# Kernel tuning notes

Measured on AMD Instinct MI355X. Metric: run time of the kernel, lower is better.

## Reference

```python
import jax, jax.numpy as jnp
import numpy as np

B, N, D = 2, 8192, 32
RADIUS2 = 0.03 ** 2
SIM_THRESH = 0.7
MIN_LEAF = 10
EPS = 1e-8


def setup_inputs() -> dict:
    key = jax.random.key(0)
    ks = jax.random.split(key, 5)
    # points scaled to [0, 0.4)^3 so the 0.03 radius finds a few neighbors per point
    points = jax.random.uniform(ks[0], (B, N, 3), dtype=jnp.float32) * 0.4
    embeddings = jax.random.normal(ks[1], (B, N, D), dtype=jnp.float32)
    leaf_mask = jax.random.randint(ks[2], (B, N), 0, 2).astype(jnp.int32)
    # consistency_net: Linear(2D -> D), ReLU, Linear(D -> D); stored as (in, out)
    W1 = jax.random.normal(ks[3], (2 * D, D), dtype=jnp.float32) / np.sqrt(2 * D)
    b1 = jnp.zeros((D,), dtype=jnp.float32)
    W2 = jax.random.normal(ks[4], (D, D), dtype=jnp.float32) / np.sqrt(D)
    b2 = jnp.zeros((D,), dtype=jnp.float32)
    return {"points": points, "embeddings": embeddings, "leaf_mask": leaf_mask,
            "W1": W1, "b1": b1, "W2": W2, "b2": b2}


def reference(points, embeddings, leaf_mask, W1, b1, W2, b2):
    leaf = leaf_mask > 0  # [B,N]
    # squared pairwise distances via ||a||^2 + ||b||^2 - 2 a.b (avoids [B,N,N,3])
    sq = jnp.sum(points * points, axis=-1)  # [B,N]
    d2 = sq[:, :, None] + sq[:, None, :] - 2.0 * jnp.einsum('bnc,bmc->bnm', points, points)
    nb = (d2 < RADIUS2) & leaf[:, None, :]  # neighbor j must be a leaf point
    nb_count = jnp.sum(nb, axis=-1)  # includes self when leaf[i]
    # cosine similarity with per-vector norm clamp (torch F.cosine_similarity eps)
    norms = jnp.maximum(jnp.linalg.norm(embeddings, axis=-1, keepdims=True), EPS)
    en = embeddings / norms
    sim = jnp.einsum('bnd,bmd->bnm', en, en)
    similar = nb & (sim > SIM_THRESH)
    cnt = jnp.sum(similar, axis=-1)  # [B,N]
    w = similar.astype(embeddings.dtype)
    mean_sim = jnp.einsum('bnm,bmd->bnd', w, embeddings) / jnp.maximum(cnt, 1)[..., None]
    combined = jnp.concatenate([embeddings, mean_sim], axis=-1)  # [B,N,2D]
    h = jax.nn.relu(combined @ W1 + b1)
    out = h @ W2 + b2
    batch_ok = (jnp.sum(leaf, axis=-1) >= MIN_LEAF)[:, None]  # skip batches with <10 leaves
    cond = leaf & (nb_count > 1) & (cnt > 0) & batch_ok
    return jnp.where(cond[..., None], out, embeddings)
```

## Files before the change

kernel.cpp:

```cpp
#include <hip/hip_runtime.h>

#define NPTS 8192
#define BN   16384
#define D    32
#define R2   0.0009f
#define SIMT 0.7f
#define RAD  0.03f
#define BLOCK 256
#define PBLOCK 1024
#define PWAVES 16
#define NGRP   (BN / 64)
#define ZBINS 512
#define ZSCALE 1280.0f
#define AFIELDS 34
#define CHUNK 512

#define GLOBAL_AS __attribute__((address_space(1)))
#define LDS_AS    __attribute__((address_space(3)))

__device__ __forceinline__ void g2lds16(const void* g, void* l) {
  __builtin_amdgcn_global_load_lds((const GLOBAL_AS void*)g, (LDS_AS void*)l,
                                   16, 0, 0);
}

__global__ __launch_bounds__(BLOCK) void prep_kernel(
    const float* __restrict__ pts, const float* __restrict__ emb,
    const int* __restrict__ leaf,
    int* __restrict__ histA, int* __restrict__ histL,
    unsigned* __restrict__ done,
    int* __restrict__ rsA, int* __restrict__ rsL,
    int* __restrict__ curA, int* __restrict__ curL,
    float4* __restrict__ sortedA, int* __restrict__ permA,
    float4* __restrict__ pts4L, float* __restrict__ invL,
    float* __restrict__ embL) {
  const int p = blockIdx.x * BLOCK + threadIdx.x;
  const float x = pts[3 * p + 0];
  const float y = pts[3 * p + 1];
  const float z = pts[3 * p + 2];
  const float sq = x * x + y * y + z * z;
  int bin = (int)(z * ZSCALE); if (bin > ZBINS - 1) bin = ZBINS - 1;
  const int b = p >> 13;
  const int lf = leaf[p] > 0;
  atomicAdd(&histA[b * ZBINS + bin], 1);
  if (lf) atomicAdd(&histL[b * ZBINS + bin], 1);

  float4 er[D / 4];
  float ss = 0.f;
  {
    const float4* __restrict__ e4 = (const float4*)(emb + (size_t)p * D);
#pragma unroll
    for (int i = 0; i < D / 4; ++i) {
      er[i] = e4[i];
      ss += er[i].x * er[i].x + er[i].y * er[i].y +
            er[i].z * er[i].z + er[i].w * er[i].w;
    }
  }
  const float inv = 1.0f / fmaxf(sqrtf(ss), 1e-8f);

  __shared__ int islast;
  __threadfence();
  if (threadIdx.x == 0) {
    const unsigned t = __hip_atomic_fetch_add(&done[0], 1u, __ATOMIC_ACQ_REL,
                                              __HIP_MEMORY_SCOPE_AGENT);
    islast = (t == gridDim.x - 1);
  }
  __syncthreads();

  if (islast) {
    const int wv = threadIdx.x >> 6;
    const int lane = threadIdx.x & 63;
    const int sb = wv & 1;
    const int* __restrict__ h = (wv < 2) ? histA : histL;
    int* __restrict__ rs = (wv < 2) ? rsA : rsL;
    int* __restrict__ cu = (wv < 2) ? curA : curL;
    int carry = 0;
    for (int c = 0; c < ZBINS / 64; ++c) {
      const int idx = c * 64 + lane;
      const int v = __hip_atomic_load(&h[sb * ZBINS + idx], __ATOMIC_RELAXED,
                                      __HIP_MEMORY_SCOPE_AGENT);
      int incl = v;
#pragma unroll
      for (int off = 1; off < 64; off <<= 1) {
        const int t = __shfl_up(incl, off);
        if (lane >= off) incl += t;
      }
      const int excl = carry + incl - v;
      rs[sb * (ZBINS + 1) + idx] = excl;
      cu[sb * ZBINS + idx] = excl;
      carry += __shfl(incl, 63);
    }
    if (lane == 0) rs[sb * (ZBINS + 1) + ZBINS] = carry;
    __threadfence();
    __syncthreads();
    if (threadIdx.x == 0)
      __hip_atomic_store(&done[1], 1u, __ATOMIC_RELEASE,
                         __HIP_MEMORY_SCOPE_AGENT);
  } else {
    if (threadIdx.x == 0) {
      while (__hip_atomic_load(&done[1], __ATOMIC_ACQUIRE,
                               __HIP_MEMORY_SCOPE_AGENT) == 0)
        __builtin_amdgcn_s_sleep(8);
    }
    __syncthreads();
  }

  const int dst = b * NPTS + atomicAdd(&curA[b * ZBINS + bin], 1);
  sortedA[dst] = make_float4(x, y, z, lf ? inv : -inv);
  permA[dst] = p;

  if (lf) {
    const int dl = b * NPTS + atomicAdd(&curL[b * ZBINS + bin], 1);
    pts4L[dl] = make_float4(x, y, z, 0.5f * (sq - R2));
    invL[dl] = inv;
    float4* __restrict__ d4 = (float4*)(embL + (size_t)dl * D);
#pragma unroll
    for (int k = 0; k < D / 4; ++k) d4[k] = er[k];
  }
}

__global__ __launch_bounds__(PBLOCK) void pair_kernel(
    const float4* __restrict__ sortedA, const int* __restrict__ permA,
    const float4* __restrict__ pts4L, const float* __restrict__ invL,
    const float* __restrict__ embL, const float* __restrict__ emb,
    const int* __restrict__ rsL,
    const float* __restrict__ W1, const float* __restrict__ b1,
    const float* __restrict__ W2, const float* __restrict__ b2,
    float* __restrict__ out) {
  const int ig   = blockIdx.x;
  const int b    = ig >> 7;
  const int lane = threadIdx.x & 63;
  const int wv   = threadIdx.x >> 6;
  const int sg   = ig * 64 + lane;

  __shared__ __align__(16) float4 ptsS[2][CHUNK];
  __shared__ __align__(16) float4 eiS4[64 * 8];
  __shared__ float invIS[64];
  __shared__ int   queueS[PWAVES][128];
  __shared__ float red[AFIELDS][64];
  for (int t = threadIdx.x; t < AFIELDS * 64; t += PBLOCK)
    (&red[0][0])[t] = 0.f;

  const float4 A = sortedA[sg];
  const float inv_i = fabsf(A.w);
  const float mhsq = -0.5f * (A.x * A.x + A.y * A.y + A.z * A.z);
  const int p = permA[sg];

  if (wv == 0) {
    const float4* __restrict__ e4 = (const float4*)(emb + (size_t)p * D);
#pragma unroll
    for (int k = 0; k < D / 4; ++k) eiS4[lane * 8 + (k ^ (lane & 7))] = e4[k];
    invIS[lane] = inv_i;
  }

  float zmin = A.z, zmax = A.z;
#pragma unroll
  for (int off = 1; off < 64; off <<= 1) {
    zmin = fminf(zmin, __shfl_xor(zmin, off));
    zmax = fmaxf(zmax, __shfl_xor(zmax, off));
  }
  int klo = (int)((zmin - RAD) * ZSCALE) - 1; if (klo < 0) klo = 0;
  int khi = (int)((zmax + RAD) * ZSCALE) + 1; if (khi > ZBINS - 1) khi = ZBINS - 1;
  klo = __builtin_amdgcn_readfirstlane(klo);
  khi = __builtin_amdgcn_readfirstlane(khi);
  const int jlo = b * NPTS + rsL[b * (ZBINS + 1) + klo];
  const int jhi = b * NPTS + rsL[b * (ZBINS + 1) + khi + 1];
  const int len = jhi - jlo;

  float nbc = 0.f;
  int qtail = 0, qdone = 0;

  const float4* __restrict__ embQ = (const float4*)embL;

  auto drain = [&](int n) {
    if (lane < n) {
      const int e  = queueS[wv][(qdone + lane) & 127];
      const int il = e & 63;
      const int j  = e >> 6;
      float4 bv[D / 4];
#pragma unroll
      for (int k = 0; k < D / 4; ++k) bv[k] = embQ[(size_t)j * 8 + k];
      const float invj = invL[j];
      float s0 = 0.f, s1 = 0.f, s2 = 0.f, s3 = 0.f;
#pragma unroll
      for (int k = 0; k < D / 4; ++k) {
        const float4 av = eiS4[il * 8 + (k ^ (il & 7))];
        s0 = fmaf(av.x, bv[k].x, s0);
        s1 = fmaf(av.y, bv[k].y, s1);
        s2 = fmaf(av.z, bv[k].z, s2);
        s3 = fmaf(av.w, bv[k].w, s3);
      }
      const float sim = ((s0 + s1) + (s2 + s3)) * invIS[il] * invj;
      if (sim > SIMT) {
        atomicAdd(&red[1][il], 1.0f);
#pragma unroll
        for (int k = 0; k < D / 4; ++k) {
          atomicAdd(&red[2 + 4 * k + 0][il], bv[k].x);
          atomicAdd(&red[2 + 4 * k + 1][il], bv[k].y);
          atomicAdd(&red[2 + 4 * k + 2][il], bv[k].z);
          atomicAdd(&red[2 + 4 * k + 3][il], bv[k].w);
        }
      }
    }
    qdone += n;
  };

  auto stage = [&](int buf, int base, int L) {
    for (int t0 = wv * 64; t0 < L; t0 += PWAVES * 64)
      g2lds16((const char*)pts4L + (((size_t)(base + t0 + lane)) << 4),
              &ptsS[buf][t0]);
  };

  auto process = [&](int buf, int jbase, int L) {
    const int s0 = (L * wv) / PWAVES;
    const int s1 = (L * (wv + 1)) / PWAVES;
    if (s0 >= s1) return;
    float4 c = ptsS[buf][s0];
    for (int jl = s0; jl < s1; ++jl) {
      const float4 cn = ptsS[buf][(jl + 1 < s1) ? (jl + 1) : s0];
      const float t = fmaf(A.z, c.z, fmaf(A.y, c.y, fmaf(A.x, c.x, mhsq)));
      const bool hit = t > c.w;
      const unsigned long long m = __ballot(hit);
      if (m) {
        if (hit) {
          nbc += 1.0f;
          const int below = __popcll(m & ((1ull << lane) - 1ull));
          queueS[wv][(qtail + below) & 127] = ((jbase + jl) << 6) | lane;
        }
        qtail += (int)__popcll(m);
        if (qtail - qdone >= 64) drain(64);
      }
      c = cn;
    }
  };

  const int nch = (len + CHUNK - 1) / CHUNK;
  if (nch > 0) stage(0, jlo, (len < CHUNK) ? len : CHUNK);
  __syncthreads();
  for (int k = 0; k < nch; ++k) {
    const int cur = k & 1;
    if (k + 1 < nch) {
      const int base = jlo + (k + 1) * CHUNK;
      const int L = (jhi - base < CHUNK) ? (jhi - base) : CHUNK;
      stage(cur ^ 1, base, L);
    }
    const int base = jlo + k * CHUNK;
    const int Lc = (jhi - base < CHUNK) ? (jhi - base) : CHUNK;
    process(cur, base, Lc);
    __syncthreads();
  }
  drain(qtail - qdone);

  if (nbc != 0.f) atomicAdd(&red[0][lane], nbc);
  __syncthreads();

  if (threadIdx.x < 64) {
    const float tnbc = red[0][lane];
    const float tcnt = red[1][lane];
    const float rinv = 1.0f / fmaxf(tcnt, 1.0f);

    float e[D];
#pragma unroll
    for (int k = 0; k < D / 4; ++k) {
      const float4 v = eiS4[lane * 8 + (k ^ (lane & 7))];
      e[4 * k + 0] = v.x; e[4 * k + 1] = v.y;
      e[4 * k + 2] = v.z; e[4 * k + 3] = v.w;
    }

    float h[D];
#pragma unroll
    for (int k = 0; k < D; ++k) h[k] = b1[k];
    for (int d = 0; d < D; ++d) {
      const float c = e[d];
      const float* __restrict__ w = W1 + (size_t)d * D;
#pragma unroll
      for (int k = 0; k < D; ++k) h[k] = fmaf(c, w[k], h[k]);
    }
    for (int d = 0; d < D; ++d) {
      const float c = red[2 + d][lane] * rinv;
      const float* __restrict__ w = W1 + (size_t)(D + d) * D;
#pragma unroll
      for (int k = 0; k < D; ++k) h[k] = fmaf(c, w[k], h[k]);
    }
#pragma unroll
    for (int k = 0; k < D; ++k) h[k] = fmaxf(h[k], 0.f);

    float o[D];
#pragma unroll
    for (int m = 0; m < D; ++m) o[m] = b2[m];
    for (int k = 0; k < D; ++k) {
      const float c = h[k];
      const float* __restrict__ w = W2 + (size_t)k * D;
#pragma unroll
      for (int m = 0; m < D; ++m) o[m] = fmaf(c, w[m], o[m]);
    }

    const bool lf = A.w > 0.f;
    const int nleaf = rsL[b * (ZBINS + 1) + ZBINS];
    const bool cond = lf && (tnbc >= 2.0f) && (tcnt >= 1.0f) && (nleaf >= 10);

    float4* outr = (float4*)(out + (size_t)p * D);
#pragma unroll
    for (int i = 0; i < D / 4; ++i) {
      float4 v;
      if (cond) { v.x = o[4*i+0]; v.y = o[4*i+1]; v.z = o[4*i+2]; v.w = o[4*i+3]; }
      else      { v.x = e[4*i+0]; v.y = e[4*i+1]; v.z = e[4*i+2]; v.w = e[4*i+3]; }
      outr[i] = v;
    }
  }
}

extern "C" void kernel_launch(void* const* d_in, const int* in_sizes, int n_in,
                              void* d_out, int out_size, void* d_ws, size_t ws_size,
                              hipStream_t stream) {
  (void)in_sizes; (void)n_in; (void)out_size; (void)ws_size;
  const float* pts  = (const float*)d_in[0];
  const float* emb  = (const float*)d_in[1];
  const int*   leaf = (const int*)d_in[2];
  const float* W1   = (const float*)d_in[3];
  const float* b1   = (const float*)d_in[4];
  const float* W2   = (const float*)d_in[5];
  const float* b2   = (const float*)d_in[6];
  float* out = (float*)d_out;

  char* ws = (char*)d_ws;
  size_t off = 0;
  auto alloc = [&](size_t bytes) { void* r = ws + off; off = (off + bytes + 15) & ~(size_t)15; return r; };

  float4*   sortedA = (float4*)alloc((size_t)BN * 16);
  int*      permA   = (int*)alloc((size_t)BN * 4);
  float4*   pts4L   = (float4*)alloc((size_t)(BN + CHUNK) * 16);
  float*    invL    = (float*)alloc((size_t)(BN + CHUNK) * 4);
  float*    embL    = (float*)alloc((size_t)(BN + CHUNK) * D * 4);
  int*      rsA     = (int*)alloc(2 * (ZBINS + 1) * 4);
  int*      rsL     = (int*)alloc(2 * (ZBINS + 1) * 4);
  int*      curA    = (int*)alloc(2 * ZBINS * 4);
  int*      curL    = (int*)alloc(2 * ZBINS * 4);
  int*      histA   = (int*)alloc(2 * ZBINS * 4);
  int*      histL   = (int*)alloc(2 * ZBINS * 4);
  unsigned* done    = (unsigned*)alloc(16);

  hipMemsetAsync(histA, 0, 2 * (2 * ZBINS * 4) + 16, stream);
  prep_kernel<<<BN / BLOCK, BLOCK, 0, stream>>>(
      pts, emb, leaf, histA, histL, done, rsA, rsL, curA, curL,
      sortedA, permA, pts4L, invL, embL);
  pair_kernel<<<NGRP, PBLOCK, 0, stream>>>(
      sortedA, permA, pts4L, invL, embL, emb, rsL,
      W1, b1, W2, b2, out);
}
```

Before: 117.6 us.

## Make pair kernel persistent with 32-point groups and two candidate rows per wave step

The pair kernel becomes persistent: a grid of 256 blocks pulls work items from a global atomic counter. Each work item is a group of 32 sorted query points instead of 64. Each wave tests two candidate rows per iteration, one per 32-lane half, so the narrower z-band still fills all 64 lanes of the ballot. This aims to cut wasted candidate scanning and balance load across blocks. Separately, the prep kernel's last-block detection swaps a threadfence plus acq_rel atomic for a block barrier plus relaxed atomic, which weakens the memory-ordering guarantees before the histogram scan.

```diff
diff --git a/kernel.cpp b/kernel.cpp
--- a/kernel.cpp
+++ b/kernel.cpp
@@ -9,7 +9,9 @@
 #define BLOCK 256
 #define PBLOCK 1024
 #define PWAVES 16
-#define NGRP   (BN / 64)
+#define PGRID  256
+#define ISZ    32
+#define NGRP2  (BN / ISZ)
 #define ZBINS 512
 #define ZSCALE 1280.0f
 #define AFIELDS 34
@@ -58,9 +60,9 @@
   const float inv = 1.0f / fmaxf(sqrtf(ss), 1e-8f);
 
   __shared__ int islast;
-  __threadfence();
+  __syncthreads();
   if (threadIdx.x == 0) {
-    const unsigned t = __hip_atomic_fetch_add(&done[0], 1u, __ATOMIC_ACQ_REL,
+    const unsigned t = __hip_atomic_fetch_add(&done[0], 1u, __ATOMIC_RELAXED,
                                               __HIP_MEMORY_SCOPE_AGENT);
     islast = (t == gridDim.x - 1);
   }
@@ -125,186 +127,195 @@
     const int* __restrict__ rsL,
     const float* __restrict__ W1, const float* __restrict__ b1,
     const float* __restrict__ W2, const float* __restrict__ b2,
-    float* __restrict__ out) {
-  const int ig   = blockIdx.x;
-  const int b    = ig >> 7;
+    int* __restrict__ gctr, float* __restrict__ out) {
   const int lane = threadIdx.x & 63;
   const int wv   = threadIdx.x >> 6;
-  const int sg   = ig * 64 + lane;
+  const int il   = lane & 31;
+  const int rp   = lane >> 5;
 
   __shared__ __align__(16) float4 ptsS[2][CHUNK];
-  __shared__ __align__(16) float4 eiS4[64 * 8];
-  __shared__ float invIS[64];
+  __shared__ __align__(16) float4 eiS4[ISZ * 8];
+  __shared__ float invIS[ISZ];
   __shared__ int   queueS[PWAVES][128];
-  __shared__ float red[AFIELDS][64];
-  for (int t = threadIdx.x; t < AFIELDS * 64; t += PBLOCK)
-    (&red[0][0])[t] = 0.f;
-
-  const float4 A = sortedA[sg];
-  const float inv_i = fabsf(A.w);
-  const float mhsq = -0.5f * (A.x * A.x + A.y * A.y + A.z * A.z);
-  const int p = permA[sg];
-
-  if (wv == 0) {
-    const float4* __restrict__ e4 = (const float4*)(emb + (size_t)p * D);
-#pragma unroll
-    for (int k = 0; k < D / 4; ++k) eiS4[lane * 8 + (k ^ (lane & 7))] = e4[k];
-    invIS[lane] = inv_i;
-  }
-
-  float zmin = A.z, zmax = A.z;
-#pragma unroll
-  for (int off = 1; off < 64; off <<= 1) {
-    zmin = fminf(zmin, __shfl_xor(zmin, off));
-    zmax = fmaxf(zmax, __shfl_xor(zmax, off));
-  }
-  int klo = (int)((zmin - RAD) * ZSCALE) - 1; if (klo < 0) klo = 0;
-  int khi = (int)((zmax + RAD) * ZSCALE) + 1; if (khi > ZBINS - 1) khi = ZBINS - 1;
-  klo = __builtin_amdgcn_readfirstlane(klo);
-  khi = __builtin_amdgcn_readfirstlane(khi);
-  const int jlo = b * NPTS + rsL[b * (ZBINS + 1) + klo];
-  const int jhi = b * NPTS + rsL[b * (ZBINS + 1) + khi + 1];
-  const int len = jhi - jlo;
-
-  float nbc = 0.f;
-  int qtail = 0, qdone = 0;
+  __shared__ float red[AFIELDS][ISZ];
+  __shared__ int   gS;
 
   const float4* __restrict__ embQ = (const float4*)embL;
 
-  auto drain = [&](int n) {
-    if (lane < n) {
-      const int e  = queueS[wv][(qdone + lane) & 127];
-      const int il = e & 63;
-      const int j  = e >> 6;
-      float4 bv[D / 4];
-#pragma unroll
-      for (int k = 0; k < D / 4; ++k) bv[k] = embQ[(size_t)j * 8 + k];
-      const float invj = invL[j];
-      float s0 = 0.f, s1 = 0.f, s2 = 0.f, s3 = 0.f;
+  for (;;) {
+    if (threadIdx.x == 0) gS = atomicAdd(gctr, 1);
+    __syncthreads();
+    const int g = gS;
+    if (g >= NGRP2) break;
+
+    for (int t = threadIdx.x; t < AFIELDS * ISZ; t += PBLOCK)
+      (&red[0][0])[t] = 0.f;
+
+    const int b  = g >> 8;
+    const int sg = g * ISZ + il;
+    const float4 A = sortedA[sg];
+    const float inv_i = fabsf(A.w);
+    const float mhsq = -0.5f * (A.x * A.x + A.y * A.y + A.z * A.z);
+    const int p = permA[sg];
+
+    if (wv == 0 && lane < ISZ) {
+      const float4* __restrict__ e4 = (const float4*)(emb + (size_t)p * D);
+#pragma unroll
+      for (int k = 0; k < D / 4; ++k) eiS4[il * 8 + (k ^ (il & 7))] = e4[k];
+      invIS[il] = inv_i;
+    }
+
+    float zmin = A.z, zmax = A.z;
+#pragma unroll
+    for (int off = 1; off < 64; off <<= 1) {
+      zmin = fminf(zmin, __shfl_xor(zmin, off));
+      zmax = fmaxf(zmax, __shfl_xor(zmax, off));
+    }
+    int klo = (int)((zmin - RAD) * ZSCALE) - 1; if (klo < 0) klo = 0;
+    int khi = (int)((zmax + RAD) * ZSCALE) + 1; if (khi > ZBINS - 1) khi = ZBINS - 1;
+    klo = __builtin_amdgcn_readfirstlane(klo);
+    khi = __builtin_amdgcn_readfirstlane(khi);
+    const int jlo = b * NPTS + rsL[b * (ZBINS + 1) + klo];
+    const int jhi = b * NPTS + rsL[b * (ZBINS + 1) + khi + 1];
+    const int len = jhi - jlo;
+
+    float nbc = 0.f;
+    int qtail = 0, qdone = 0;
+
+    auto drain = [&](int n) {
+      if (lane < n) {
+        const int e  = queueS[wv][(qdone + lane) & 127];
+        const int ii = e & 31;
+        const int j  = e >> 5;
+        float4 bv[D / 4];
+#pragma unroll
+        for (int k = 0; k < D / 4; ++k) bv[k] = embQ[(size_t)j * 8 + k];
+        const float invj = invL[j];
+        float s0 = 0.f, s1 = 0.f, s2 = 0.f, s3 = 0.f;
+#pragma unroll
+        for (int k = 0; k < D / 4; ++k) {
+          const float4 av = eiS4[ii * 8 + (k ^ (ii & 7))];
+          s0 = fmaf(av.x, bv[k].x, s0);
+          s1 = fmaf(av.y, bv[k].y, s1);
+          s2 = fmaf(av.z, bv[k].z, s2);
+          s3 = fmaf(av.w, bv[k].w, s3);
+        }
+        const float sim = ((s0 + s1) + (s2 + s3)) * invIS[ii] * invj;
+        if (sim > SIMT) {
+          atomicAdd(&red[1][ii], 1.0f);
+#pragma unroll
+          for (int k = 0; k < D / 4; ++k) {
+            atomicAdd(&red[2 + 4 * k + 0][ii], bv[k].x);
+            atomicAdd(&red[2 + 4 * k + 1][ii], bv[k].y);
+            atomicAdd(&red[2 + 4 * k + 2][ii], bv[k].z);
+            atomicAdd(&red[2 + 4 * k + 3][ii], bv[k].w);
+          }
+        }
+      }
+      qdone += n;
+    };
+
+    auto stage = [&](int buf, int base, int L) {
+      for (int t0 = wv * 64; t0 < L; t0 += PWAVES * 64)
+        g2lds16((const char*)pts4L + (((size_t)(base + t0 + lane)) << 4),
+                &ptsS[buf][t0]);
+    };
+
+    auto process = [&](int buf, int jbase, int L) {
+      const int s0 = (L * wv) / PWAVES;
+      const int s1 = (L * (wv + 1)) / PWAVES;
+      for (int jl = s0; jl < s1; jl += 2) {
+        const int row = jl + rp;
+        const bool inb = row < s1;
+        const float4 c = ptsS[buf][inb ? row : s0];
+        const float t = fmaf(A.z, c.z, fmaf(A.y, c.y, fmaf(A.x, c.x, mhsq)));
+        const bool hit = inb && (t > c.w);
+        const unsigned long long m = __ballot(hit);
+        if (m) {
+          if (hit) {
+            nbc += 1.0f;
+            const int below = __popcll(m & ((1ull << lane) - 1ull));
+            queueS[wv][(qtail + below) & 127] = ((jbase + row) << 5) | il;
+          }
+          qtail += (int)__popcll(m);
+          if (qtail - qdone >= 64) drain(64);
+        }
+      }
+    };
+
+    const int nch = (len + CHUNK - 1) / CHUNK;
+    if (nch > 0) stage(0, jlo, (len < CHUNK) ? len : CHUNK);
+    __syncthreads();
+    for (int k = 0; k < nch; ++k) {
+      const int cur = k & 1;
+      if (k + 1 < nch) {
+        const int base = jlo + (k + 1) * CHUNK;
+        const int L = (jhi - base < CHUNK) ? (jhi - base) : CHUNK;
+        stage(cur ^ 1, base, L);
+      }
+      const int base = jlo + k * CHUNK;
+      const int Lc = (jhi - base < CHUNK) ? (jhi - base) : CHUNK;
+      process(cur, base, Lc);
+      __syncthreads();
+    }
+    drain(qtail - qdone);
+
+    if (nbc != 0.f) atomicAdd(&red[0][il], nbc);
+    __syncthreads();
+
+    if (threadIdx.x < ISZ) {
+      const float tnbc = red[0][lane];
+      const float tcnt = red[1][lane];
+      const float rinv = 1.0f / fmaxf(tcnt, 1.0f);
+
+      float e[D];
 #pragma unroll
       for (int k = 0; k < D / 4; ++k) {
-        const float4 av = eiS4[il * 8 + (k ^ (il & 7))];
-        s0 = fmaf(av.x, bv[k].x, s0);
-        s1 = fmaf(av.y, bv[k].y, s1);
-        s2 = fmaf(av.z, bv[k].z, s2);
-        s3 = fmaf(av.w, bv[k].w, s3);
-      }
-      const float sim = ((s0 + s1) + (s2 + s3)) * invIS[il] * invj;
-      if (sim > SIMT) {
-        atomicAdd(&red[1][il], 1.0f);
-#pragma unroll
-        for (int k = 0; k < D / 4; ++k) {
-          atomicAdd(&red[2 + 4 * k + 0][il], bv[k].x);
-          atomicAdd(&red[2 + 4 * k + 1][il], bv[k].y);
-          atomicAdd(&red[2 + 4 * k + 2][il], bv[k].z);
-          atomicAdd(&red[2 + 4 * k + 3][il], bv[k].w);
-        }
-      }
-    }
-    qdone += n;
-  };
-
-  auto stage = [&](int buf, int base, int L) {
-    for (int t0 = wv * 64; t0 < L; t0 += PWAVES * 64)
-      g2lds16((const char*)pts4L + (((size_t)(base + t0 + lane)) << 4),
-              &ptsS[buf][t0]);
-  };
-
-  auto process = [&](int buf, int jbase, int L) {
-    const int s0 = (L * wv) / PWAVES;
-    const int s1 = (L * (wv + 1)) / PWAVES;
-    if (s0 >= s1) return;
-    float4 c = ptsS[buf][s0];
-    for (int jl = s0; jl < s1; ++jl) {
-      const float4 cn = ptsS[buf][(jl + 1 < s1) ? (jl + 1) : s0];
-      const float t = fmaf(A.z, c.z, fmaf(A.y, c.y, fmaf(A.x, c.x, mhsq)));
-      const bool hit = t > c.w;
-      const unsigned long long m = __ballot(hit);
-      if (m) {
-        if (hit) {
-          nbc += 1.0f;
-          const int below = __popcll(m & ((1ull << lane) - 1ull));
-          queueS[wv][(qtail + below) & 127] = ((jbase + jl) << 6) | lane;
-        }
-        qtail += (int)__popcll(m);
-        if (qtail - qdone >= 64) drain(64);
-      }
-      c = cn;
-    }
-  };
-
-  const int nch = (len + CHUNK - 1) / CHUNK;
-  if (nch > 0) stage(0, jlo, (len < CHUNK) ? len : CHUNK);
-  __syncthreads();
-  for (int k = 0; k < nch; ++k) {
-    const int cur = k & 1;
-    if (k + 1 < nch) {
-      const int base = jlo + (k + 1) * CHUNK;
-      const int L = (jhi - base < CHUNK) ? (jhi - base) : CHUNK;
-      stage(cur ^ 1, base, L);
-    }
-    const int base = jlo + k * CHUNK;
-    const int Lc = (jhi - base < CHUNK) ? (jhi - base) : CHUNK;
-    process(cur, base, Lc);
-    __syncthreads();
-  }
-  drain(qtail - qdone);
-
-  if (nbc != 0.f) atomicAdd(&red[0][lane], nbc);
-  __syncthreads();
-
-  if (threadIdx.x < 64) {
-    const float tnbc = red[0][lane];
-    const float tcnt = red[1][lane];
-    const float rinv = 1.0f / fmaxf(tcnt, 1.0f);
-
-    float e[D];
-#pragma unroll
-    for (int k = 0; k < D / 4; ++k) {
-      const float4 v = eiS4[lane * 8 + (k ^ (lane & 7))];
-      e[4 * k + 0] = v.x; e[4 * k + 1] = v.y;
-      e[4 * k + 2] = v.z; e[4 * k + 3] = v.w;
-    }
-
-    float h[D];
-#pragma unroll
-    for (int k = 0; k < D; ++k) h[k] = b1[k];
-    for (int d = 0; d < D; ++d) {
-      const float c = e[d];
-      const float* __restrict__ w = W1 + (size_t)d * D;
-#pragma unroll
-      for (int k = 0; k < D; ++k) h[k] = fmaf(c, w[k], h[k]);
-    }
-    for (int d = 0; d < D; ++d) {
-      const float c = red[2 + d][lane] * rinv;
-      const float* __restrict__ w = W1 + (size_t)(D + d) * D;
-#pragma unroll
-      for (int k = 0; k < D; ++k) h[k] = fmaf(c, w[k], h[k]);
-    }
-#pragma unroll
-    for (int k = 0; k < D; ++k) h[k] = fmaxf(h[k], 0.f);
-
-    float o[D];
-#pragma unroll
-    for (int m = 0; m < D; ++m) o[m] = b2[m];
-    for (int k = 0; k < D; ++k) {
-      const float c = h[k];
-      const float* __restrict__ w = W2 + (size_t)k * D;
-#pragma unroll
-      for (int m = 0; m < D; ++m) o[m] = fmaf(c, w[m], o[m]);
-    }
-
-    const bool lf = A.w > 0.f;
-    const int nleaf = rsL[b * (ZBINS + 1) + ZBINS];
-    const bool cond = lf && (tnbc >= 2.0f) && (tcnt >= 1.0f) && (nleaf >= 10);
-
-    float4* outr = (float4*)(out + (size_t)p * D);
-#pragma unroll
-    for (int i = 0; i < D / 4; ++i) {
-      float4 v;
-      if (cond) { v.x = o[4*i+0]; v.y = o[4*i+1]; v.z = o[4*i+2]; v.w = o[4*i+3]; }
-      else      { v.x = e[4*i+0]; v.y = e[4*i+1]; v.z = e[4*i+2]; v.w = e[4*i+3]; }
-      outr[i] = v;
+        const float4 v = eiS4[lane * 8 + (k ^ (lane & 7))];
+        e[4 * k + 0] = v.x; e[4 * k + 1] = v.y;
+        e[4 * k + 2] = v.z; e[4 * k + 3] = v.w;
+      }
+
+      float h[D];
+#pragma unroll
+      for (int k = 0; k < D; ++k) h[k] = b1[k];
+      for (int d = 0; d < D; ++d) {
+        const float c = e[d];
+        const float* __restrict__ w = W1 + (size_t)d * D;
+#pragma unroll
+        for (int k = 0; k < D; ++k) h[k] = fmaf(c, w[k], h[k]);
+      }
+      for (int d = 0; d < D; ++d) {
+        const float c = red[2 + d][lane] * rinv;
+        const float* __restrict__ w = W1 + (size_t)(D + d) * D;
+#pragma unroll
+        for (int k = 0; k < D; ++k) h[k] = fmaf(c, w[k], h[k]);
+      }
+#pragma unroll
+      for (int k = 0; k < D; ++k) h[k] = fmaxf(h[k], 0.f);
+
+      float o[D];
+#pragma unroll
+      for (int m = 0; m < D; ++m) o[m] = b2[m];
+      for (int k = 0; k < D; ++k) {
+        const float c = h[k];
+        const float* __restrict__ w = W2 + (size_t)k * D;
+#pragma unroll
+        for (int m = 0; m < D; ++m) o[m] = fmaf(c, w[m], o[m]);
+      }
+
+      const bool lf = A.w > 0.f;
+      const int nleaf = rsL[b * (ZBINS + 1) + ZBINS];
+      const bool cond = lf && (tnbc >= 2.0f) && (tcnt >= 1.0f) && (nleaf >= 10);
+
+      float4* outr = (float4*)(out + (size_t)p * D);
+#pragma unroll
+      for (int i = 0; i < D / 4; ++i) {
+        float4 v;
+        if (cond) { v.x = o[4*i+0]; v.y = o[4*i+1]; v.z = o[4*i+2]; v.w = o[4*i+3]; }
+        else      { v.x = e[4*i+0]; v.y = e[4*i+1]; v.z = e[4*i+2]; v.w = e[4*i+3]; }
+        outr[i] = v;
+      }
     }
   }
 }
@@ -338,12 +349,13 @@
   int*      histA   = (int*)alloc(2 * ZBINS * 4);
   int*      histL   = (int*)alloc(2 * ZBINS * 4);
   unsigned* done    = (unsigned*)alloc(16);
-
-  hipMemsetAsync(histA, 0, 2 * (2 * ZBINS * 4) + 16, stream);
+  int*      gctr    = (int*)alloc(16);
+
+  hipMemsetAsync(histA, 0, 2 * (2 * ZBINS * 4) + 32, stream);
   prep_kernel<<<BN / BLOCK, BLOCK, 0, stream>>>(
       pts, emb, leaf, histA, histL, done, rsA, rsL, curA, curL,
       sortedA, permA, pts4L, invL, embL);
-  pair_kernel<<<NGRP, PBLOCK, 0, stream>>>(
+  pair_kernel<<<PGRID, PBLOCK, 0, stream>>>(
       sortedA, permA, pts4L, invL, embL, emb, rsL,
-      W1, b1, W2, b2, out);
+      W1, b1, W2, b2, gctr, out);
 }
```

Measured after the change: 157.4 us. +33.9%, slower.
